# Kernel optimization log

Measured on AMD Instinct MI355X. Metric: run time of the kernel, lower is better.

## Reference

```python
import jax, jax.numpy as jnp
import numpy as np

TEMPERATURE = 0.05
EPS = 1e-8  # F.cosine_similarity default eps


def setup_inputs() -> dict:
    key = jax.random.key(0)
    k1, k2 = jax.random.split(key)
    N, D = 8192, 256
    return {
        "query_embeddings": jax.random.normal(k1, (N, D), dtype=jnp.float32),
        "pos_embeddings": jax.random.normal(k2, (N, D), dtype=jnp.float32),
    }


def _normalize(x):
    # matches F.cosine_similarity: x / max(||x||, eps)
    norm = jnp.sqrt(jnp.sum(x * x, axis=-1, keepdims=True))
    return x / jnp.maximum(norm, EPS)


def reference(query_embeddings, pos_embeddings):
    q = _normalize(query_embeddings)  # [N, D]
    p = _normalize(pos_embeddings)    # [N, D]
    # cosine similarity matrix via GEMM instead of (N,N,D) broadcast
    sim = jnp.einsum("nd,md->nm", q, p) / TEMPERATURE  # [N, N]
    # cross-entropy with labels = arange(N): loss_i = logsumexp(sim_i) - sim_ii
    logz = jax.nn.logsumexp(sim, axis=-1)  # [N]
    diag = jnp.diagonal(sim)               # [N]
    loss = jnp.mean(logz - diag)
    return loss
```

## Files before the change

### kernel.cpp

```cpp
#include <hip/hip_runtime.h>
#include <hip/hip_bf16.h>

#define NROWS 8192
#define DDIM  256
#define INV_TEMP 20.0f

typedef __attribute__((ext_vector_type(8))) short bf16x8;
typedef __attribute__((ext_vector_type(4))) float f32x4;

__device__ static inline void async16(const void* g, void* l) {
    __builtin_amdgcn_global_load_lds(
        (const __attribute__((address_space(1))) void*)g,
        (__attribute__((address_space(3))) void*)l, 16, 0, 0);
}

__global__ __launch_bounds__(256) void norm_diag_kernel(
    const float* __restrict__ q, const float* __restrict__ p,
    unsigned short* __restrict__ qn, unsigned short* __restrict__ pn,
    float* __restrict__ diag, int* __restrict__ tickets)
{
    if (blockIdx.x == 0 && threadIdx.x == 0) tickets[0] = 0;

    const int row  = (blockIdx.x << 2) + (threadIdx.x >> 6);
    const int lane = threadIdx.x & 63;

    const float4 qv = ((const float4*)(q + (size_t)row * DDIM))[lane];
    const float4 pv = ((const float4*)(p + (size_t)row * DDIM))[lane];

    float sq = qv.x*qv.x + qv.y*qv.y + qv.z*qv.z + qv.w*qv.w;
    float sp = pv.x*pv.x + pv.y*pv.y + pv.z*pv.z + pv.w*pv.w;
    #pragma unroll
    for (int m = 1; m < 64; m <<= 1) {
        sq += __shfl_xor(sq, m);
        sp += __shfl_xor(sp, m);
    }
    const float qs = 1.0f / fmaxf(sqrtf(sq), 1e-8f);
    const float ps = 1.0f / fmaxf(sqrtf(sp), 1e-8f);

    const float qx = qv.x*qs, qy = qv.y*qs, qz = qv.z*qs, qw = qv.w*qs;
    const float px = pv.x*ps, py = pv.y*ps, pz = pv.z*ps, pw = pv.w*ps;

    float d = qx*px + qy*py + qz*pz + qw*pw;
    #pragma unroll
    for (int m = 1; m < 64; m <<= 1) d += __shfl_xor(d, m);
    if (lane == 0) diag[row] = d * INV_TEMP;

    union { unsigned short u16[4]; uint2 v; } uq, up;
    {
        __hip_bfloat16 b;
        b = __float2bfloat16(qx); uq.u16[0] = *(unsigned short*)&b;
        b = __float2bfloat16(qy); uq.u16[1] = *(unsigned short*)&b;
        b = __float2bfloat16(qz); uq.u16[2] = *(unsigned short*)&b;
        b = __float2bfloat16(qw); uq.u16[3] = *(unsigned short*)&b;
        b = __float2bfloat16(px); up.u16[0] = *(unsigned short*)&b;
        b = __float2bfloat16(py); up.u16[1] = *(unsigned short*)&b;
        b = __float2bfloat16(pz); up.u16[2] = *(unsigned short*)&b;
        b = __float2bfloat16(pw); up.u16[3] = *(unsigned short*)&b;
    }
    *(uint2*)(qn + (size_t)row * DDIM + lane * 4) = uq.v;
    *(uint2*)(pn + (size_t)row * DDIM + lane * 4) = up.v;
}

__global__ __launch_bounds__(512, 2) void simexp_kernel(
    const unsigned short* __restrict__ qn,
    const unsigned short* __restrict__ pn,
    float* __restrict__ part)
{
    __shared__ unsigned char lds[3 * 32768];

    const int tid  = threadIdx.x;
    const int lane = tid & 63;
    const int w    = tid >> 6;
    const int wr   = w >> 2;
    const int wc   = w & 3;
    const int quad = lane >> 4;
    const int l16  = lane & 15;

    const int L   = blockIdx.y * 32 + blockIdx.x;
    const int xcd = L & 7;
    const int c   = L >> 3;
    const int rowblk = xcd * 4 + (c & 3);
    const int colblk = c >> 2;
    const int rowbase = rowblk * 256;
    const int colbase = colblk * 256;

    const unsigned short* gA0 = qn + (size_t)(rowbase + (2*w  )*16 + l16) * DDIM + quad * 8;
    const unsigned short* gA1 = qn + (size_t)(rowbase + (2*w+1)*16 + l16) * DDIM + quad * 8;
    const unsigned short* gB0 = pn + (size_t)(colbase + (2*w  )*16 + l16) * DDIM + quad * 8;
    const unsigned short* gB1 = pn + (size_t)(colbase + (2*w+1)*16 + l16) * DDIM + quad * 8;

    f32x4 acc[8][4];
    #pragma unroll
    for (int i = 0; i < 8; ++i)
        #pragma unroll
        for (int j = 0; j < 4; ++j) acc[i][j] = (f32x4)0.0f;

#define STAGE(buf, ks) do {                                             \
        unsigned char* _b = lds + (buf) * 32768;                        \
        async16(gA0 + (ks) * 32, _b +         (2*w    ) * 1024);        \
        async16(gA1 + (ks) * 32, _b +         (2*w + 1) * 1024);        \
        async16(gB0 + (ks) * 32, _b + 16384 + (2*w    ) * 1024);        \
        async16(gB1 + (ks) * 32, _b + 16384 + (2*w + 1) * 1024);        \
    } while (0)

    STAGE(0, 0);
    STAGE(1, 1);
    asm volatile("s_waitcnt vmcnt(4)" ::: "memory");
    __builtin_amdgcn_s_barrier();
    asm volatile("" ::: "memory");

    #pragma unroll
    for (int ks = 0; ks < 8; ++ks) {
        if (ks < 6) STAGE((ks + 2) % 3, ks + 2);

        const unsigned char* ba = lds + (ks % 3) * 32768;
        bf16x8 af[8], bf[4];
        #pragma unroll
        for (int i = 0; i < 8; ++i)
            af[i] = *(const bf16x8*)(ba + (wr*8 + i) * 1024 + quad * 256 + l16 * 16);
        #pragma unroll
        for (int j = 0; j < 4; ++j)
            bf[j] = *(const bf16x8*)(ba + 16384 + (wc*4 + j) * 1024 + quad * 256 + l16 * 16);

        #pragma unroll
        for (int i = 0; i < 8; ++i)
            #pragma unroll
            for (int j = 0; j < 4; ++j)
                acc[i][j] = __builtin_amdgcn_mfma_f32_16x16x32_bf16(
                    af[i], bf[j], acc[i][j], 0, 0, 0);

        if (ks < 7) {
            if (ks < 6) { asm volatile("s_waitcnt vmcnt(4)" ::: "memory"); }
            else        { asm volatile("s_waitcnt vmcnt(0)" ::: "memory"); }
            __builtin_amdgcn_s_barrier();
            asm volatile("" ::: "memory");
        }
    }
#undef STAGE

    __syncthreads();
    float* red = (float*)lds;

    #pragma unroll
    for (int i = 0; i < 8; ++i)
        #pragma unroll
        for (int r = 0; r < 4; ++r) {
            float s = __expf(acc[i][0][r] * INV_TEMP)
                    + __expf(acc[i][1][r] * INV_TEMP)
                    + __expf(acc[i][2][r] * INV_TEMP)
                    + __expf(acc[i][3][r] * INV_TEMP);
            s += __shfl_xor(s, 1);
            s += __shfl_xor(s, 2);
            s += __shfl_xor(s, 4);
            s += __shfl_xor(s, 8);
            if (l16 == 0)
                red[wc * 256 + wr * 128 + i * 16 + quad * 4 + r] = s;
        }
    __syncthreads();

    if (tid < 256)
        part[(size_t)colblk * NROWS + rowbase + tid] =
            red[tid] + red[256 + tid] + red[512 + tid] + red[768 + tid];
}

__global__ __launch_bounds__(128) void rowsum_final_kernel(
    const float* __restrict__ part, const float* __restrict__ diag,
    float* __restrict__ loss_part, int* __restrict__ tickets,
    float* __restrict__ out)
{
    const int row = blockIdx.x * 128 + threadIdx.x;
    float s = 0.0f;
    #pragma unroll 4
    for (int cb = 0; cb < 32; ++cb)
        s += part[(size_t)cb * NROWS + row];
    float v = logf(s) - diag[row];

    #pragma unroll
    for (int m = 1; m < 64; m <<= 1) v += __shfl_xor(v, m);
    __shared__ float wsum[2];
    __shared__ int swin;
    if ((threadIdx.x & 63) == 0) wsum[threadIdx.x >> 6] = v;
    __syncthreads();
    if (threadIdx.x == 0) {
        __hip_atomic_store(&loss_part[blockIdx.x], wsum[0] + wsum[1],
            __ATOMIC_RELEASE, __HIP_MEMORY_SCOPE_AGENT);
        swin = __hip_atomic_fetch_add(&tickets[0], 1,
                   __ATOMIC_ACQ_REL, __HIP_MEMORY_SCOPE_AGENT);
    }
    __syncthreads();
    if (swin != 63) return;

    if (threadIdx.x < 64) {
        float x = __hip_atomic_load(&loss_part[threadIdx.x],
                      __ATOMIC_RELAXED, __HIP_MEMORY_SCOPE_AGENT);
        #pragma unroll
        for (int m = 1; m < 64; m <<= 1) x += __shfl_xor(x, m);
        if (threadIdx.x == 0) out[0] = x * (1.0f / NROWS);
    }
}

extern "C" void kernel_launch(void* const* d_in, const int* in_sizes, int n_in,
                              void* d_out, int out_size, void* d_ws, size_t ws_size,
                              hipStream_t stream)
{
    const float* q = (const float*)d_in[0];
    const float* p = (const float*)d_in[1];

    char* ws = (char*)d_ws;
    unsigned short* qn   = (unsigned short*)ws;
    unsigned short* pn   = (unsigned short*)(ws + (size_t)NROWS*DDIM*2);
    float* part      = (float*)(ws + 2*(size_t)NROWS*DDIM*2);
    float* diag      = part + 32 * (size_t)NROWS;
    float* loss_part = diag + NROWS;
    int*   tickets   = (int*)(loss_part + 64);

    norm_diag_kernel<<<NROWS/4, 256, 0, stream>>>(q, p, qn, pn, diag, tickets);

    dim3 grid(32, 32);
    simexp_kernel<<<grid, 512, 0, stream>>>(qn, pn, part);

    rowsum_final_kernel<<<64, 128, 0, stream>>>(part, diag, loss_part,
                                                tickets, (float*)d_out);
}
```

Measured before the change: 131.1 us.

## Restructure GEMM K-loop into double-buffered 64-wide tiles with phased prefetch and setprio

Replaces the triple-buffered 32-wide K pipeline with two 64-wide K buffers, each split into two 32-wide phases. The next stage's async loads are issued after the LDS fragment reads but before the barrier, and the MFMA cluster is wrapped in s_setprio so the math runs at raised wave priority. The goal is to overlap global-to-LDS loads with the MFMAs and to cut barrier stalls. LDS use rises to 128 KB per block, which, together with launch_bounds(512,2), may reduce the number of resident blocks per CU.

```diff
diff --git a/kernel.cpp b/kernel.cpp
--- a/kernel.cpp
+++ b/kernel.cpp
@@ -66,7 +66,7 @@
     const unsigned short* __restrict__ pn,
     float* __restrict__ part)
 {
-    __shared__ unsigned char lds[3 * 32768];
+    __shared__ unsigned char lds[131072];
 
     const int tid  = threadIdx.x;
     const int lane = tid & 63;
@@ -75,6 +75,7 @@
     const int wc   = w & 3;
     const int quad = lane >> 4;
     const int l16  = lane & 15;
+    const int qoff = lane * 16;
 
     const int L   = blockIdx.y * 32 + blockIdx.x;
     const int xcd = L & 7;
@@ -95,48 +96,69 @@
         #pragma unroll
         for (int j = 0; j < 4; ++j) acc[i][j] = (f32x4)0.0f;
 
-#define STAGE(buf, ks) do {                                             \
-        unsigned char* _b = lds + (buf) * 32768;                        \
-        async16(gA0 + (ks) * 32, _b +         (2*w    ) * 1024);        \
-        async16(gA1 + (ks) * 32, _b +         (2*w + 1) * 1024);        \
-        async16(gB0 + (ks) * 32, _b + 16384 + (2*w    ) * 1024);        \
-        async16(gB1 + (ks) * 32, _b + 16384 + (2*w + 1) * 1024);        \
+#define STG(SKT, SPH) do {                                              \
+        unsigned char* _d = lds + ((SKT) & 1) * 65536 + (SPH) * 1024;   \
+        const int _ko = (SKT) * 64 + (SPH) * 32;                        \
+        async16(gA0 + _ko, _d +         (2*w    ) * 2048);              \
+        async16(gA1 + _ko, _d +         (2*w + 1) * 2048);              \
+        async16(gB0 + _ko, _d + 32768 + (2*w    ) * 2048);              \
+        async16(gB1 + _ko, _d + 32768 + (2*w + 1) * 2048);              \
     } while (0)
 
-    STAGE(0, 0);
-    STAGE(1, 1);
-    asm volatile("s_waitcnt vmcnt(4)" ::: "memory");
+#define MFMA_CLUSTER() do {                                             \
+        __builtin_amdgcn_s_setprio(1);                                  \
+        _Pragma("unroll")                                               \
+        for (int i = 0; i < 8; ++i)                                     \
+            _Pragma("unroll")                                           \
+            for (int j = 0; j < 4; ++j)                                 \
+                acc[i][j] = __builtin_amdgcn_mfma_f32_16x16x32_bf16(    \
+                    af[i], bf[j], acc[i][j], 0, 0, 0);                  \
+        __builtin_amdgcn_s_setprio(0);                                  \
+    } while (0)
+
+#define PHASE(BUF, PH, STGSTMT, VMSTR) {                                \
+        bf16x8 af[8], bf[4];                                            \
+        const unsigned char* _ba = lds + (BUF) * 65536 + (PH) * 1024;   \
+        _Pragma("unroll")                                               \
+        for (int i = 0; i < 8; ++i)                                     \
+            af[i] = *(const bf16x8*)(_ba + (wr*8 + i) * 2048 + qoff);   \
+        _Pragma("unroll")                                               \
+        for (int j = 0; j < 4; ++j)                                     \
+            bf[j] = *(const bf16x8*)(_ba + 32768 + (wc*4 + j) * 2048 + qoff); \
+        STGSTMT;                                                        \
+        asm volatile(VMSTR ::: "memory");                               \
+        asm volatile("s_waitcnt lgkmcnt(0)" ::: "memory");              \
+        __builtin_amdgcn_s_barrier();                                   \
+        asm volatile("" ::: "memory");                                  \
+        MFMA_CLUSTER();                                                 \
+    }
+
+    STG(0, 0); STG(0, 1); STG(1, 0);
+    asm volatile("s_waitcnt vmcnt(8)" ::: "memory");
     __builtin_amdgcn_s_barrier();
     asm volatile("" ::: "memory");
 
-    #pragma unroll
-    for (int ks = 0; ks < 8; ++ks) {
-        if (ks < 6) STAGE((ks + 2) % 3, ks + 2);
-
-        const unsigned char* ba = lds + (ks % 3) * 32768;
+    PHASE(0, 0, STG(1, 1), "s_waitcnt vmcnt(8)")
+    PHASE(0, 1, STG(2, 0), "s_waitcnt vmcnt(8)")
+    PHASE(1, 0, STG(2, 1), "s_waitcnt vmcnt(8)")
+    PHASE(1, 1, STG(3, 0), "s_waitcnt vmcnt(8)")
+    PHASE(0, 0, STG(3, 1), "s_waitcnt vmcnt(8)")
+    PHASE(0, 1, ((void)0),  "s_waitcnt vmcnt(4)")
+    PHASE(1, 0, ((void)0),  "s_waitcnt vmcnt(0)")
+    {
         bf16x8 af[8], bf[4];
+        const unsigned char* _ba = lds + 65536 + 1024;
         #pragma unroll
         for (int i = 0; i < 8; ++i)
-            af[i] = *(const bf16x8*)(ba + (wr*8 + i) * 1024 + quad * 256 + l16 * 16);
+            af[i] = *(const bf16x8*)(_ba + (wr*8 + i) * 2048 + qoff);
         #pragma unroll
         for (int j = 0; j < 4; ++j)
-            bf[j] = *(const bf16x8*)(ba + 16384 + (wc*4 + j) * 1024 + quad * 256 + l16 * 16);
-
-        #pragma unroll
-        for (int i = 0; i < 8; ++i)
-            #pragma unroll
-            for (int j = 0; j < 4; ++j)
-                acc[i][j] = __builtin_amdgcn_mfma_f32_16x16x32_bf16(
-                    af[i], bf[j], acc[i][j], 0, 0, 0);
-
-        if (ks < 7) {
-            if (ks < 6) { asm volatile("s_waitcnt vmcnt(4)" ::: "memory"); }
-            else        { asm volatile("s_waitcnt vmcnt(0)" ::: "memory"); }
-            __builtin_amdgcn_s_barrier();
-            asm volatile("" ::: "memory");
-        }
-    }
-#undef STAGE
+            bf[j] = *(const bf16x8*)(_ba + 32768 + (wc*4 + j) * 2048 + qoff);
+        MFMA_CLUSTER();
+    }
+#undef PHASE
+#undef MFMA_CLUSTER
+#undef STG
 
     __syncthreads();
     float* red = (float*)lds;
```

After: 133.1 us. Within noise of the previous version (+1.5%).

## Fuse normalize, GEMM-exp and row reduction into one cooperative persistent kernel

Applied to the files above, without the earlier changes.

Replaces the three separate launches with a single cooperative kernel of 256 blocks. Each block first normalizes 32 rows, then after a grid sync computes four 256x256 sim-exp tiles sequentially, then reduces partial sums and the loss across two more grid syncs. This removes launch gaps and the ticket-based final reduction. In exchange it adds grid-wide barrier costs, and only 256 blocks are resident instead of 1024, so each block runs four tiles serially with no overlap across tiles and may leave the GPU less fully occupied.

```diff
diff --git a/kernel.cpp b/kernel.cpp
--- a/kernel.cpp
+++ b/kernel.cpp
@@ -1,5 +1,8 @@
 #include <hip/hip_runtime.h>
 #include <hip/hip_bf16.h>
+#include <hip/hip_cooperative_groups.h>
+
+namespace cg = cooperative_groups;
 
 #define NROWS 8192
 #define DDIM  256
@@ -14,86 +17,95 @@
         (__attribute__((address_space(3))) void*)l, 16, 0, 0);
 }
 
-__global__ __launch_bounds__(256) void norm_diag_kernel(
+__global__ __launch_bounds__(512, 2) void simcse_fused_kernel(
     const float* __restrict__ q, const float* __restrict__ p,
     unsigned short* __restrict__ qn, unsigned short* __restrict__ pn,
-    float* __restrict__ diag, int* __restrict__ tickets)
-{
-    if (blockIdx.x == 0 && threadIdx.x == 0) tickets[0] = 0;
-
-    const int row  = (blockIdx.x << 2) + (threadIdx.x >> 6);
-    const int lane = threadIdx.x & 63;
-
-    const float4 qv = ((const float4*)(q + (size_t)row * DDIM))[lane];
-    const float4 pv = ((const float4*)(p + (size_t)row * DDIM))[lane];
-
-    float sq = qv.x*qv.x + qv.y*qv.y + qv.z*qv.z + qv.w*qv.w;
-    float sp = pv.x*pv.x + pv.y*pv.y + pv.z*pv.z + pv.w*pv.w;
-    #pragma unroll
-    for (int m = 1; m < 64; m <<= 1) {
-        sq += __shfl_xor(sq, m);
-        sp += __shfl_xor(sp, m);
-    }
-    const float qs = 1.0f / fmaxf(sqrtf(sq), 1e-8f);
-    const float ps = 1.0f / fmaxf(sqrtf(sp), 1e-8f);
-
-    const float qx = qv.x*qs, qy = qv.y*qs, qz = qv.z*qs, qw = qv.w*qs;
-    const float px = pv.x*ps, py = pv.y*ps, pz = pv.z*ps, pw = pv.w*ps;
-
-    float d = qx*px + qy*py + qz*pz + qw*pw;
-    #pragma unroll
-    for (int m = 1; m < 64; m <<= 1) d += __shfl_xor(d, m);
-    if (lane == 0) diag[row] = d * INV_TEMP;
-
-    union { unsigned short u16[4]; uint2 v; } uq, up;
-    {
-        __hip_bfloat16 b;
-        b = __float2bfloat16(qx); uq.u16[0] = *(unsigned short*)&b;
-        b = __float2bfloat16(qy); uq.u16[1] = *(unsigned short*)&b;
-        b = __float2bfloat16(qz); uq.u16[2] = *(unsigned short*)&b;
-        b = __float2bfloat16(qw); uq.u16[3] = *(unsigned short*)&b;
-        b = __float2bfloat16(px); up.u16[0] = *(unsigned short*)&b;
-        b = __float2bfloat16(py); up.u16[1] = *(unsigned short*)&b;
-        b = __float2bfloat16(pz); up.u16[2] = *(unsigned short*)&b;
-        b = __float2bfloat16(pw); up.u16[3] = *(unsigned short*)&b;
-    }
-    *(uint2*)(qn + (size_t)row * DDIM + lane * 4) = uq.v;
-    *(uint2*)(pn + (size_t)row * DDIM + lane * 4) = up.v;
-}
-
-__global__ __launch_bounds__(512, 2) void simexp_kernel(
-    const unsigned short* __restrict__ qn,
-    const unsigned short* __restrict__ pn,
-    float* __restrict__ part)
+    float* __restrict__ diag,
+    float* __restrict__ part,
+    float* __restrict__ loss_part,
+    float* __restrict__ out)
 {
     __shared__ unsigned char lds[3 * 32768];
-
+    cg::grid_group grid = cg::this_grid();
+
+    const int b    = blockIdx.x;
     const int tid  = threadIdx.x;
     const int lane = tid & 63;
     const int w    = tid >> 6;
+
+    #pragma unroll 1
+    for (int k = 0; k < 4; ++k) {
+        const int row = b * 32 + w * 4 + k;
+
+        const float4 qv = ((const float4*)(q + (size_t)row * DDIM))[lane];
+        const float4 pv = ((const float4*)(p + (size_t)row * DDIM))[lane];
+
+        float sq = qv.x*qv.x + qv.y*qv.y + qv.z*qv.z + qv.w*qv.w;
+        float sp = pv.x*pv.x + pv.y*pv.y + pv.z*pv.z + pv.w*pv.w;
+        #pragma unroll
+        for (int m = 1; m < 64; m <<= 1) {
+            sq += __shfl_xor(sq, m);
+            sp += __shfl_xor(sp, m);
+        }
+        const float qs = 1.0f / fmaxf(sqrtf(sq), 1e-8f);
+        const float ps = 1.0f / fmaxf(sqrtf(sp), 1e-8f);
+
+        const float qx = qv.x*qs, qy = qv.y*qs, qz = qv.z*qs, qw = qv.w*qs;
+        const float px = pv.x*ps, py = pv.y*ps, pz = pv.z*ps, pw = pv.w*ps;
+
+        float d = qx*px + qy*py + qz*pz + qw*pw;
+        #pragma unroll
+        for (int m = 1; m < 64; m <<= 1) d += __shfl_xor(d, m);
+        if (lane == 0) diag[row] = d * INV_TEMP;
+
+        union { unsigned short u16[4]; uint2 v; } uq, up;
+        {
+            __hip_bfloat16 bb;
+            bb = __float2bfloat16(qx); uq.u16[0] = *(unsigned short*)&bb;
+            bb = __float2bfloat16(qy); uq.u16[1] = *(unsigned short*)&bb;
+            bb = __float2bfloat16(qz); uq.u16[2] = *(unsigned short*)&bb;
+            bb = __float2bfloat16(qw); uq.u16[3] = *(unsigned short*)&bb;
+            bb = __float2bfloat16(px); up.u16[0] = *(unsigned short*)&bb;
+            bb = __float2bfloat16(py); up.u16[1] = *(unsigned short*)&bb;
+            bb = __float2bfloat16(pz); up.u16[2] = *(unsigned short*)&bb;
+            bb = __float2bfloat16(pw); up.u16[3] = *(unsigned short*)&bb;
+        }
+        *(uint2*)(qn + (size_t)row * DDIM + lane * 4) = uq.v;
+        *(uint2*)(pn + (size_t)row * DDIM + lane * 4) = up.v;
+    }
+
+    __threadfence();
+    grid.sync();
+    __threadfence();
+
     const int wr   = w >> 2;
     const int wc   = w & 3;
     const int quad = lane >> 4;
     const int l16  = lane & 15;
 
-    const int L   = blockIdx.y * 32 + blockIdx.x;
-    const int xcd = L & 7;
-    const int c   = L >> 3;
-    const int rowblk = xcd * 4 + (c & 3);
-    const int colblk = c >> 2;
+    const int xcd    = b & 7;
+    const int ii     = b >> 3;
+    const int rowblk = xcd * 4 + (ii & 3);
+    const int colgrp = ii >> 2;
     const int rowbase = rowblk * 256;
-    const int colbase = colblk * 256;
 
     const unsigned short* gA0 = qn + (size_t)(rowbase + (2*w  )*16 + l16) * DDIM + quad * 8;
     const unsigned short* gA1 = qn + (size_t)(rowbase + (2*w+1)*16 + l16) * DDIM + quad * 8;
-    const unsigned short* gB0 = pn + (size_t)(colbase + (2*w  )*16 + l16) * DDIM + quad * 8;
-    const unsigned short* gB1 = pn + (size_t)(colbase + (2*w+1)*16 + l16) * DDIM + quad * 8;
 
     f32x4 acc[8][4];
-    #pragma unroll
-    for (int i = 0; i < 8; ++i)
-        #pragma unroll
-        for (int j = 0; j < 4; ++j) acc[i][j] = (f32x4)0.0f;
+
+    #pragma unroll 1
+    for (int t = 0; t < 4; ++t) {
+        const int colblk  = colgrp * 4 + t;
+        const int colbase = colblk * 256;
+
+        const unsigned short* gB0 = pn + (size_t)(colbase + (2*w  )*16 + l16) * DDIM + quad * 8;
+        const unsigned short* gB1 = pn + (size_t)(colbase + (2*w+1)*16 + l16) * DDIM + quad * 8;
+
+        #pragma unroll
+        for (int i = 0; i < 8; ++i)
+            #pragma unroll
+            for (int j = 0; j < 4; ++j) acc[i][j] = (f32x4)0.0f;
 
 #define STAGE(buf, ks) do {                                             \
         unsigned char* _b = lds + (buf) * 32768;                        \
@@ -103,99 +115,106 @@
         async16(gB1 + (ks) * 32, _b + 16384 + (2*w + 1) * 1024);        \
     } while (0)
 
-    STAGE(0, 0);
-    STAGE(1, 1);
-    asm volatile("s_waitcnt vmcnt(4)" ::: "memory");
-    __builtin_amdgcn_s_barrier();
-    asm volatile("" ::: "memory");
-
-    #pragma unroll
-    for (int ks = 0; ks < 8; ++ks) {
-        if (ks < 6) STAGE((ks + 2) % 3, ks + 2);
-
-        const unsigned char* ba = lds + (ks % 3) * 32768;
-        bf16x8 af[8], bf[4];
+        STAGE(0, 0);
+        STAGE(1, 1);
+        asm volatile("s_waitcnt vmcnt(4)" ::: "memory");
+        __builtin_amdgcn_s_barrier();
+        asm volatile("" ::: "memory");
+
+        #pragma unroll
+        for (int ks = 0; ks < 8; ++ks) {
+            if (ks < 6) STAGE((ks + 2) % 3, ks + 2);
+
+            const unsigned char* ba = lds + (ks % 3) * 32768;
+            bf16x8 af[8], bf[4];
+            #pragma unroll
+            for (int i = 0; i < 8; ++i)
+                af[i] = *(const bf16x8*)(ba + (wr*8 + i) * 1024 + quad * 256 + l16 * 16);
+            #pragma unroll
+            for (int j = 0; j < 4; ++j)
+                bf[j] = *(const bf16x8*)(ba + 16384 + (wc*4 + j) * 1024 + quad * 256 + l16 * 16);
+
+            #pragma unroll
+            for (int i = 0; i < 8; ++i)
+                #pragma unroll
+                for (int j = 0; j < 4; ++j)
+                    acc[i][j] = __builtin_amdgcn_mfma_f32_16x16x32_bf16(
+                        af[i], bf[j], acc[i][j], 0, 0, 0);
+
+            if (ks < 7) {
+                if (ks < 6) { asm volatile("s_waitcnt vmcnt(4)" ::: "memory"); }
+                else        { asm volatile("s_waitcnt vmcnt(0)" ::: "memory"); }
+                __builtin_amdgcn_s_barrier();
+                asm volatile("" ::: "memory");
+            }
+        }
+#undef STAGE
+
+        __syncthreads();
+        float* red = (float*)lds;
+
         #pragma unroll
         for (int i = 0; i < 8; ++i)
-            af[i] = *(const bf16x8*)(ba + (wr*8 + i) * 1024 + quad * 256 + l16 * 16);
-        #pragma unroll
-        for (int j = 0; j < 4; ++j)
-            bf[j] = *(const bf16x8*)(ba + 16384 + (wc*4 + j) * 1024 + quad * 256 + l16 * 16);
-
-        #pragma unroll
-        for (int i = 0; i < 8; ++i)
-            #pragma unroll
-            for (int j = 0; j < 4; ++j)
-                acc[i][j] = __builtin_amdgcn_mfma_f32_16x16x32_bf16(
-                    af[i], bf[j], acc[i][j], 0, 0, 0);
-
-        if (ks < 7) {
-            if (ks < 6) { asm volatile("s_waitcnt vmcnt(4)" ::: "memory"); }
-            else        { asm volatile("s_waitcnt vmcnt(0)" ::: "memory"); }
-            __builtin_amdgcn_s_barrier();
-            asm volatile("" ::: "memory");
-        }
-    }
-#undef STAGE
-
-    __syncthreads();
-    float* red = (float*)lds;
-
-    #pragma unroll
-    for (int i = 0; i < 8; ++i)
-        #pragma unroll
-        for (int r = 0; r < 4; ++r) {
-            float s = __expf(acc[i][0][r] * INV_TEMP)
-                    + __expf(acc[i][1][r] * INV_TEMP)
-                    + __expf(acc[i][2][r] * INV_TEMP)
-                    + __expf(acc[i][3][r] * INV_TEMP);
-            s += __shfl_xor(s, 1);
-            s += __shfl_xor(s, 2);
-            s += __shfl_xor(s, 4);
-            s += __shfl_xor(s, 8);
-            if (l16 == 0)
-                red[wc * 256 + wr * 128 + i * 16 + quad * 4 + r] = s;
-        }
-    __syncthreads();
-
-    if (tid < 256)
-        part[(size_t)colblk * NROWS + rowbase + tid] =
-            red[tid] + red[256 + tid] + red[512 + tid] + red[768 + tid];
-}
-
-__global__ __launch_bounds__(128) void rowsum_final_kernel(
-    const float* __restrict__ part, const float* __restrict__ diag,
-    float* __restrict__ loss_part, int* __restrict__ tickets,
-    float* __restrict__ out)
-{
-    const int row = blockIdx.x * 128 + threadIdx.x;
-    float s = 0.0f;
-    #pragma unroll 4
-    for (int cb = 0; cb < 32; ++cb)
-        s += part[(size_t)cb * NROWS + row];
-    float v = logf(s) - diag[row];
-
-    #pragma unroll
-    for (int m = 1; m < 64; m <<= 1) v += __shfl_xor(v, m);
-    __shared__ float wsum[2];
-    __shared__ int swin;
-    if ((threadIdx.x & 63) == 0) wsum[threadIdx.x >> 6] = v;
-    __syncthreads();
-    if (threadIdx.x == 0) {
-        __hip_atomic_store(&loss_part[blockIdx.x], wsum[0] + wsum[1],
-            __ATOMIC_RELEASE, __HIP_MEMORY_SCOPE_AGENT);
-        swin = __hip_atomic_fetch_add(&tickets[0], 1,
-                   __ATOMIC_ACQ_REL, __HIP_MEMORY_SCOPE_AGENT);
-    }
-    __syncthreads();
-    if (swin != 63) return;
-
-    if (threadIdx.x < 64) {
-        float x = __hip_atomic_load(&loss_part[threadIdx.x],
-                      __ATOMIC_RELAXED, __HIP_MEMORY_SCOPE_AGENT);
-        #pragma unroll
-        for (int m = 1; m < 64; m <<= 1) x += __shfl_xor(x, m);
-        if (threadIdx.x == 0) out[0] = x * (1.0f / NROWS);
+            #pragma unroll
+            for (int r = 0; r < 4; ++r) {
+                float s = __expf(acc[i][0][r] * INV_TEMP)
+                        + __expf(acc[i][1][r] * INV_TEMP)
+                        + __expf(acc[i][2][r] * INV_TEMP)
+                        + __expf(acc[i][3][r] * INV_TEMP);
+                s += __shfl_xor(s, 1);
+                s += __shfl_xor(s, 2);
+                s += __shfl_xor(s, 4);
+                s += __shfl_xor(s, 8);
+                if (l16 == 0)
+                    red[wc * 256 + wr * 128 + i * 16 + quad * 4 + r] = s;
+            }
+        __syncthreads();
+
+        if (tid < 256)
+            part[(size_t)colblk * NROWS + rowbase + tid] =
+                red[tid] + red[256 + tid] + red[512 + tid] + red[768 + tid];
+        __syncthreads();
+    }
+
+    __threadfence();
+    grid.sync();
+    __threadfence();
+
+    {
+        const int r32 = tid & 31;
+        const int sl  = tid >> 5;
+        const int row = b * 32 + r32;
+        float s = part[(size_t)(2*sl    ) * NROWS + row]
+                + part[(size_t)(2*sl + 1) * NROWS + row];
+        float* psum = (float*)lds;
+        psum[r32 * 17 + sl] = s;
+        __syncthreads();
+
+        if (tid < 32) {
+            float tot = 0.0f;
+            #pragma unroll
+            for (int s16 = 0; s16 < 16; ++s16) tot += psum[tid * 17 + s16];
+            float v = logf(tot) - diag[b * 32 + tid];
+            #pragma unroll
+            for (int m = 1; m < 32; m <<= 1) v += __shfl_xor(v, m);
+            if (tid == 0) loss_part[b] = v;
+        }
+    }
+
+    __threadfence();
+    grid.sync();
+    __threadfence();
+
+    if (b == 0) {
+        float v = (tid < 256) ? loss_part[tid] : 0.0f;
+        #pragma unroll
+        for (int m = 1; m < 64; m <<= 1) v += __shfl_xor(v, m);
+        float* ws8 = (float*)lds;
+        if (lane == 0) ws8[w] = v;
+        __syncthreads();
+        if (tid == 0)
+            out[0] = (ws8[0] + ws8[1] + ws8[2] + ws8[3] +
+                      ws8[4] + ws8[5] + ws8[6] + ws8[7]) * (1.0f / NROWS);
     }
 }
 
@@ -212,13 +231,12 @@
     float* part      = (float*)(ws + 2*(size_t)NROWS*DDIM*2);
     float* diag      = part + 32 * (size_t)NROWS;
     float* loss_part = diag + NROWS;
-    int*   tickets   = (int*)(loss_part + 64);
-
-    norm_diag_kernel<<<NROWS/4, 256, 0, stream>>>(q, p, qn, pn, diag, tickets);
-
-    dim3 grid(32, 32);
-    simexp_kernel<<<grid, 512, 0, stream>>>(qn, pn, part);
-
-    rowsum_final_kernel<<<64, 128, 0, stream>>>(part, diag, loss_part,
-                                                tickets, (float*)d_out);
+    float* outp      = (float*)d_out;
+
+    void* args[] = { (void*)&q, (void*)&p, (void*)&qn, (void*)&pn,
+                     (void*)&diag, (void*)&part, (void*)&loss_part,
+                     (void*)&outp };
+
+    hipLaunchCooperativeKernel((const void*)simcse_fused_kernel,
+                               dim3(256), dim3(512), args, 0, stream);
 }
```

New measurement: 421.1 us. +221.1%, slower.

## Fuse row-sum and final reduction into GEMM kernel via per-rowblock tickets

Applied to the files above, without the earlier changes.

Removes the separate rowsum/final kernel launch. Each GEMM block now bumps an atomic ticket for its row block, and the last of the 32 column blocks sums the partials, takes the log, subtracts the diagonal and stores a per-rowblock loss. A second ticket lets the final row block write the mean. This saves a kernel launch and its inter-kernel gap, but adds a thread fence and atomics to every GEMM block plus a serialized tail in the last block of each row.

```diff
diff --git a/kernel.cpp b/kernel.cpp
--- a/kernel.cpp
+++ b/kernel.cpp
@@ -19,7 +19,8 @@
     unsigned short* __restrict__ qn, unsigned short* __restrict__ pn,
     float* __restrict__ diag, int* __restrict__ tickets)
 {
-    if (blockIdx.x == 0 && threadIdx.x == 0) tickets[0] = 0;
+    if (blockIdx.x == 0 && threadIdx.x < 33)
+        tickets[threadIdx.x * 32] = 0;
 
     const int row  = (blockIdx.x << 2) + (threadIdx.x >> 6);
     const int lane = threadIdx.x & 63;
@@ -64,7 +65,11 @@
 __global__ __launch_bounds__(512, 2) void simexp_kernel(
     const unsigned short* __restrict__ qn,
     const unsigned short* __restrict__ pn,
-    float* __restrict__ part)
+    float* __restrict__ part,
+    const float* __restrict__ diag,
+    float* __restrict__ loss_part,
+    int* __restrict__ tickets,
+    float* __restrict__ out)
 {
     __shared__ unsigned char lds[3 * 32768];
 
@@ -161,41 +166,50 @@
     if (tid < 256)
         part[(size_t)colblk * NROWS + rowbase + tid] =
             red[tid] + red[256 + tid] + red[512 + tid] + red[768 + tid];
-}
-
-__global__ __launch_bounds__(128) void rowsum_final_kernel(
-    const float* __restrict__ part, const float* __restrict__ diag,
-    float* __restrict__ loss_part, int* __restrict__ tickets,
-    float* __restrict__ out)
-{
-    const int row = blockIdx.x * 128 + threadIdx.x;
-    float s = 0.0f;
-    #pragma unroll 4
-    for (int cb = 0; cb < 32; ++cb)
-        s += part[(size_t)cb * NROWS + row];
-    float v = logf(s) - diag[row];
-
+
+    __threadfence();
+    __syncthreads();
+    __shared__ int swin;
+    __shared__ int sdone;
+    if (tid == 0)
+        swin = __hip_atomic_fetch_add(&tickets[rowblk * 32], 1,
+                   __ATOMIC_ACQ_REL, __HIP_MEMORY_SCOPE_AGENT);
+    __syncthreads();
+    if (swin != 31) return;
+
+    float* wsum = (float*)lds;
+    float v = 0.0f;
+    if (tid < 256) {
+        const int row = rowbase + tid;
+        float s = 0.0f;
+        #pragma unroll 4
+        for (int cb = 0; cb < 32; ++cb)
+            s += __hip_atomic_load(&part[(size_t)cb * NROWS + row],
+                     __ATOMIC_RELAXED, __HIP_MEMORY_SCOPE_AGENT);
+        v = logf(s) - diag[row];
+    }
     #pragma unroll
     for (int m = 1; m < 64; m <<= 1) v += __shfl_xor(v, m);
-    __shared__ float wsum[2];
-    __shared__ int swin;
-    if ((threadIdx.x & 63) == 0) wsum[threadIdx.x >> 6] = v;
-    __syncthreads();
-    if (threadIdx.x == 0) {
-        __hip_atomic_store(&loss_part[blockIdx.x], wsum[0] + wsum[1],
+    if (lane == 0) wsum[w] = v;
+    __syncthreads();
+    if (tid == 0) {
+        __hip_atomic_store(&loss_part[rowblk],
+            wsum[0] + wsum[1] + wsum[2] + wsum[3] +
+            wsum[4] + wsum[5] + wsum[6] + wsum[7],
             __ATOMIC_RELEASE, __HIP_MEMORY_SCOPE_AGENT);
-        swin = __hip_atomic_fetch_add(&tickets[0], 1,
-                   __ATOMIC_ACQ_REL, __HIP_MEMORY_SCOPE_AGENT);
-    }
-    __syncthreads();
-    if (swin != 63) return;
-
-    if (threadIdx.x < 64) {
-        float x = __hip_atomic_load(&loss_part[threadIdx.x],
+        const int d = __hip_atomic_fetch_add(&tickets[32 * 32], 1,
+                          __ATOMIC_ACQ_REL, __HIP_MEMORY_SCOPE_AGENT);
+        sdone = (d == 31);
+    }
+    __syncthreads();
+    if (!sdone) return;
+
+    if (tid < 32) {
+        float x = __hip_atomic_load(&loss_part[tid],
                       __ATOMIC_RELAXED, __HIP_MEMORY_SCOPE_AGENT);
         #pragma unroll
-        for (int m = 1; m < 64; m <<= 1) x += __shfl_xor(x, m);
-        if (threadIdx.x == 0) out[0] = x * (1.0f / NROWS);
+        for (int m = 1; m < 32; m <<= 1) x += __shfl_xor(x, m);
+        if (tid == 0) out[0] = x * (1.0f / NROWS);
     }
 }
 
@@ -212,13 +226,11 @@
     float* part      = (float*)(ws + 2*(size_t)NROWS*DDIM*2);
     float* diag      = part + 32 * (size_t)NROWS;
     float* loss_part = diag + NROWS;
-    int*   tickets   = (int*)(loss_part + 64);
+    int*   tickets   = (int*)(loss_part + 32);
 
     norm_diag_kernel<<<NROWS/4, 256, 0, stream>>>(q, p, qn, pn, diag, tickets);
 
     dim3 grid(32, 32);
-    simexp_kernel<<<grid, 512, 0, stream>>>(qn, pn, part);
-
-    rowsum_final_kernel<<<64, 128, 0, stream>>>(part, diag, loss_part,
-                                                tickets, (float*)d_out);
-}
+    simexp_kernel<<<grid, 512, 0, stream>>>(qn, pn, part, diag, loss_part,
+                                            tickets, (float*)d_out);
+}
```

Result: slower. 266.0 us (+102.9%).
